# Optimization experiments

Hardware: AMD Instinct MI355X
Metric: run time of the kernel (lower is better)

## Reference

```python
import jax, jax.numpy as jnp
import numpy as np

B, S, H = 4096, 15, 1024
PQ, CFG = 1003, 128
IN = PQ + 5 + 10 + 3 + 3  # 1024, matches input_size in torch module
EPS = 1e-5


def lstm_cell(x, h, c, Wih, Whh, bih, bhh):
    # PyTorch LSTMCell gate order: i, f, g, o
    gates = x @ Wih.T + bih + h @ Whh.T + bhh
    i, f, g, o = jnp.split(gates, 4, axis=-1)
    c2 = jax.nn.sigmoid(f) * c + jax.nn.sigmoid(i) * jnp.tanh(g)
    h2 = jax.nn.sigmoid(o) * jnp.tanh(c2)
    return h2, c2


def setup_inputs() -> dict:
    key = jax.random.key(0)
    ks = jax.random.split(key, 16)
    g = lambda i, shape, s=0.02: jax.random.normal(ks[i], shape, jnp.float32) * s
    u = lambda i, shape: jax.random.uniform(ks[i], shape, jnp.float32, -1.0, 1.0)
    return {
        "input_p_q": jax.random.normal(ks[0], (B, S, PQ), jnp.float32),
        "input_config": jax.random.normal(ks[1], (B, S, CFG), jnp.float32),
        "input_time": jax.random.randint(ks[2], (B, S, 3), 0, 5),
        "W_cfg": g(3, (10, CFG)), "b_cfg": jnp.zeros((10,), jnp.float32),
        "emb_hour": g(4, (24, 5), 1.0),
        "emb_weekday": g(5, (8, 3), 1.0),
        "emb_season": g(6, (5, 3), 1.0),
        # init(): uniform(-1,1) weights, zero bias for the two attention layers
        "W_sa": u(7, (IN, IN + 2 * H)), "b_sa": jnp.zeros((IN,), jnp.float32),
        "Wih_s": g(8, (4 * H, IN)), "Whh_s": g(9, (4 * H, H)),
        "bih_s": jnp.zeros((4 * H,), jnp.float32), "bhh_s": jnp.zeros((4 * H,), jnp.float32),
        "Wih_t": g(10, (4 * H, H)), "Whh_t": g(11, (4 * H, H)),
        "bih_t": jnp.zeros((4 * H,), jnp.float32), "bhh_t": jnp.zeros((4 * H,), jnp.float32),
        "W_ta": u(12, (1, 3 * H)), "b_ta": jnp.zeros((1,), jnp.float32),
        "bn_gamma": jnp.ones((S,), jnp.float32), "bn_beta": jnp.zeros((S,), jnp.float32),
        "Wih_d": g(13, (4, H)), "Whh_d": g(14, (4, 1)),
        "bih_d": jnp.zeros((4,), jnp.float32), "bhh_d": jnp.zeros((4,), jnp.float32),
    }


def reference(input_p_q, input_config, input_time,
              W_cfg, b_cfg, emb_hour, emb_weekday, emb_season,
              W_sa, b_sa, Wih_s, Whh_s, bih_s, bhh_s,
              Wih_t, Whh_t, bih_t, bhh_t, W_ta, b_ta,
              bn_gamma, bn_beta, Wih_d, Whh_d, bih_d, bhh_d):
    cfg = input_config @ W_cfg.T + b_cfg                       # [B,S,10]
    hr = emb_hour[input_time[:, :, 0]]                         # [B,S,5]
    wd = emb_weekday[input_time[:, :, 1]]                      # [B,S,3]
    sn = emb_season[input_time[:, :, 2]]                       # [B,S,3]
    inputs = jnp.concatenate([input_p_q, cfg, hr, wd, sn], axis=2)  # [B,S,IN]

    Bsz, Ssz = inputs.shape[0], inputs.shape[1]
    Hd = Whh_s.shape[1]
    h0 = jnp.zeros((Bsz, Hd), inputs.dtype)

    # ---- spatial encoder with per-step attention gating ----
    def step1(carry, x):
        h, c = carry
        score = jnp.tanh(jnp.concatenate([h, c, x], axis=1) @ W_sa.T + b_sa)
        h2, c2 = lstm_cell(x * score, h, c, Wih_s, Whh_s, bih_s, bhh_s)
        return (h2, c2), h2

    _, mid = jax.lax.scan(step1, (h0, h0), jnp.swapaxes(inputs, 0, 1))  # [S,B,H]
    mid = jnp.swapaxes(mid, 0, 1)                                      # [B,S,H]

    # ---- BatchNorm1d(15) in training mode: channels = sequence dim ----
    mu = mid.mean(axis=(0, 2), keepdims=True)
    var = mid.var(axis=(0, 2), keepdims=True)  # biased variance, as torch uses for normalization
    mid = (mid - mu) * jax.lax.rsqrt(var + EPS) * bn_gamma[None, :, None] + bn_beta[None, :, None]

    # ---- temporal encoder with post-step attention score ----
    def step2(carry, x):
        h, c = carry
        h2, c2 = lstm_cell(x, h, c, Wih_t, Whh_t, bih_t, bhh_t)
        att = jnp.tanh(jnp.concatenate([h2, c2, x], axis=1) @ W_ta.T + b_ta)  # [B,1]
        return (h2, c2), (h2, att)

    _, (outs, att2) = jax.lax.scan(step2, (h0, h0), jnp.swapaxes(mid, 0, 1))
    outs = jnp.swapaxes(outs, 0, 1)   # [B,S,H]
    att2 = jnp.swapaxes(att2, 0, 1)   # [B,S,1]

    # ---- decoder nn.LSTM (batch_first=False!) scans over the BATCH axis ----
    hd0 = jnp.zeros((Ssz, 1), outs.dtype)

    def step3(carry, x):
        h, c = carry
        h2, c2 = lstm_cell(x, h, c, Wih_d, Whh_d, bih_d, bhh_d)
        return (h2, c2), h2

    _, out1d = jax.lax.scan(step3, (hd0, hd0), outs)  # [B,S,1]

    sm = jax.nn.softmax(att2, axis=1)  # [B,S,1]
    # bmm(out1d^T [B,1,S], sm [B,S,1]) -> [B,1,1]
    out = jnp.einsum('bs,bs->b', out1d[:, :, 0], sm[:, :, 0])[:, None, None]
    return out
```

## Files before the change

kernel.cpp:

```cpp
#include <hip/hip_runtime.h>

#define AS1 __attribute__((address_space(1)))
#define AS3 __attribute__((address_space(3)))

typedef __attribute__((ext_vector_type(8))) _Float16 f16x8;
typedef __attribute__((ext_vector_type(4))) float f32x4;

static constexpr int BATCH = 4096;
static constexpr int SEQ   = 15;

__device__ __forceinline__ float h2f(unsigned short u) {
  return (float)__builtin_bit_cast(_Float16, u);
}
__device__ __forceinline__ unsigned short f2h(float f) {
  return __builtin_bit_cast(unsigned short, (_Float16)f);
}
__device__ __forceinline__ float frcp(float x) { return __builtin_amdgcn_rcpf(x); }
__device__ __forceinline__ float sigm(float x)  { return frcp(1.0f + __expf(-x)); }
__device__ __forceinline__ float tanhx(float x) { return 1.0f - 2.0f * frcp(1.0f + __expf(2.0f * x)); }

template<int STAGE>
__global__ __launch_bounds__(512, 2)
void gemm_lstm256(const unsigned short* A0, int lda0, int K0,
                  const unsigned short* A1, int lda1,
                  const unsigned short* Bw, int K,
                  const float* ib, float* Cst,
                  unsigned short* P0, unsigned short* P1, unsigned short* P2,
                  float* F0)
{
  __shared__ unsigned short lds[2][2][16384];
  const int tid  = threadIdx.x;
  const int wid  = tid >> 6;
  const int lane = tid & 63;
  const int wr = wid >> 2;
  const int wc = wid & 3;
  const int NT = K >> 6;

  const int bid = blockIdx.y * gridDim.x + blockIdx.x;
  const int cpx = (gridDim.x * gridDim.y) >> 3;
  const int swz = (bid & 7) * cpx + (bid >> 3);
  const int row0 = (swz / gridDim.x) * 256;
  const int col0 = (swz % gridDim.x) * 256;

  auto stage_half = [&](int bb, int mat, int hh, int kt) {
    const int k0 = kt * 64;
    const unsigned short* Ap; int lda, kc, rb;
    if (mat == 0) {
      if (k0 < K0) { Ap = A0; lda = lda0; kc = k0; }
      else         { Ap = A1; lda = lda1; kc = k0 - K0; }
      rb = row0;
    } else { Ap = Bw; lda = K; kc = k0; rb = col0; }
#pragma unroll
    for (int i = 0; i < 2; ++i) {
      const int x  = (tid + i * 512) * 16;
      const int xs = x ^ (((x >> 9) & 1) << 5);
      const int r  = hh * 128 + (xs >> 7);
      const int cb = xs & 127;
      const unsigned short* src = Ap + (size_t)(rb + r) * lda + kc + (cb >> 1);
      __builtin_amdgcn_global_load_lds((const AS1 void*)src,
          (AS3 void*)((char*)&lds[bb][mat][0] + hh * 16384 + wid * 1024 + i * 8192),
          16, 0, 0);
    }
  };

  const int frow = lane & 15;
  const int axor = ((lane >> 2) & 1) << 5;
  const int abase = ((((wr * 128 + frow) << 7) + (((lane >> 4) & 3) << 4))) ^ axor;
  const int bbase = ((((wc * 64  + frow) << 7) + (((lane >> 4) & 3) << 4))) ^ axor;

  const f32x4 zero = {0.f, 0.f, 0.f, 0.f};
  f32x4 acc[8][4];
#pragma unroll
  for (int i = 0; i < 8; ++i)
#pragma unroll
    for (int j = 0; j < 4; ++j) acc[i][j] = zero;

  stage_half(0, 0, 0, 0);
  stage_half(0, 0, 1, 0);
  stage_half(0, 1, 0, 0);
  stage_half(0, 1, 1, 0);
  if (NT > 1) { stage_half(1, 1, 0, 1); stage_half(1, 1, 1, 1); }
  asm volatile("s_waitcnt vmcnt(4)" ::: "memory");
  __builtin_amdgcn_s_barrier();

#define DO_PHASE(MB, STG, VMW)                                                        \
  {                                                                                   \
    const f16x8 a0 = *(const f16x8*)(ldsA + abase + (MB)     * 2048);                 \
    const f16x8 a1 = *(const f16x8*)(ldsA + abase + (MB)     * 2048 + 64);            \
    const f16x8 a2 = *(const f16x8*)(ldsA + abase + (MB + 1) * 2048);                 \
    const f16x8 a3 = *(const f16x8*)(ldsA + abase + (MB + 1) * 2048 + 64);            \
    STG;                                                                              \
    __builtin_amdgcn_s_barrier();                                                     \
    asm volatile("s_waitcnt lgkmcnt(0)" ::: "memory");                                \
    __builtin_amdgcn_sched_barrier(0);                                                \
    __builtin_amdgcn_s_setprio(1);                                                    \
    _Pragma("unroll")                                                                 \
    for (int n = 0; n < 4; ++n) {                                                     \
      acc[MB][n]     = __builtin_amdgcn_mfma_f32_16x16x32_f16(a0, bv[n][0], acc[MB][n],     0, 0, 0); \
      acc[MB][n]     = __builtin_amdgcn_mfma_f32_16x16x32_f16(a1, bv[n][1], acc[MB][n],     0, 0, 0); \
      acc[MB + 1][n] = __builtin_amdgcn_mfma_f32_16x16x32_f16(a2, bv[n][0], acc[MB + 1][n], 0, 0, 0); \
      acc[MB + 1][n] = __builtin_amdgcn_mfma_f32_16x16x32_f16(a3, bv[n][1], acc[MB + 1][n], 0, 0, 0); \
    }                                                                                 \
    __builtin_amdgcn_s_setprio(0);                                                    \
    VMW;                                                                              \
    __builtin_amdgcn_s_barrier();                                                     \
  }

  for (int kt = 0; kt < NT; ++kt) {
    const int cur = kt & 1;
    const char* ldsA = (const char*)&lds[cur][0][0];
    const char* ldsB = (const char*)&lds[cur][1][0];
    f16x8 bv[4][2];
#pragma unroll
    for (int n = 0; n < 4; ++n) {
      bv[n][0] = *(const f16x8*)(ldsB + bbase + n * 2048);
      bv[n][1] = *(const f16x8*)(ldsB + bbase + n * 2048 + 64);
    }
    DO_PHASE(0, { if (kt + 1 < NT) stage_half(cur ^ 1, 0, 0, kt + 1); }, { (void)0; });
    DO_PHASE(2, { if (kt + 1 < NT) stage_half(cur ^ 1, 0, 1, kt + 1); }, { (void)0; });
    DO_PHASE(4, { if (kt + 2 < NT) stage_half(cur,     1, 0, kt + 2); }, { (void)0; });
    DO_PHASE(6, { if (kt + 2 < NT) stage_half(cur,     1, 1, kt + 2); },
             { if (kt >= NT - 2) { asm volatile("s_waitcnt vmcnt(0)" ::: "memory"); }
               else              { asm volatile("s_waitcnt vmcnt(4)" ::: "memory"); } });
  }
#undef DO_PHASE

  float* xw = ((float*)&lds[0][0][0]) + wid * 256;
  const int cs = lane & 3;
  const int er = (lane >> 4) << 2;
  const int uq = (lane >> 2) & 3;

  float cold[8][4];
#pragma unroll
  for (int mi = 0; mi < 8; ++mi)
#pragma unroll
    for (int ni = 0; ni < 4; ++ni) {
      const int R = row0 + wr * 128 + mi * 16 + er + cs;
      const int U = ((col0 + wc * 64 + ni * 16) >> 2) + uq;
      cold[mi][ni] = Cst[(size_t)R * 1024 + U];
    }

#pragma unroll
  for (int mi = 0; mi < 8; ++mi)
#pragma unroll
    for (int ni = 0; ni < 4; ++ni) {
      __builtin_amdgcn_wave_barrier();
      *(f32x4*)(xw + lane * 4) = acc[mi][ni];
      __builtin_amdgcn_wave_barrier();
      __builtin_amdgcn_sched_barrier(0);
      const int qb = (lane & 60) * 4;
      const float g0 = xw[qb + 0  + cs];
      const float g1 = xw[qb + 4  + cs];
      const float g2 = xw[qb + 8  + cs];
      const float g3 = xw[qb + 12 + cs];
      __builtin_amdgcn_wave_barrier();
      const int R = row0 + wr * 128 + mi * 16 + er + cs;
      const int U = ((col0 + wc * 64 + ni * 16) >> 2) + uq;
      const f32x4 b4 = *(const f32x4*)(ib + 4 * U);
      const float gi = g0 + b4[0];
      const float gf = g1 + b4[1];
      const float gg = g2 + b4[2];
      const float go = g3 + b4[3];
      const size_t off = (size_t)R * 1024 + U;
      const float cn = sigm(gf) * cold[mi][ni] + sigm(gi) * tanhx(gg);
      const float hn = sigm(go) * tanhx(cn);
      Cst[off] = cn;
      const unsigned short hb = f2h(hn);
      if (STAGE == 1) {
        P0[(size_t)R * 2048 + U]        = hb;
        P0[(size_t)R * 2048 + 1024 + U] = f2h(cn);
        P1[(size_t)R * 2048 + 1024 + U] = hb;
        P2[off] = hb;
      } else {
        F0[off] = hn;
        P0[off] = hb;
      }
    }
}

__global__ __launch_bounds__(512, 2)
void gemm_score256(const unsigned short* A0, int lda0, int K0,
                   const unsigned short* A1, int lda1,
                   const unsigned short* Bw, int K,
                   const float* bias, const unsigned short* X,
                   unsigned short* OutG)
{
  __shared__ unsigned short lds[2][24576];
  const int tid  = threadIdx.x;
  const int wid  = tid >> 6;
  const int lane = tid & 63;
  const int wr = wid >> 2;
  const int wc = wid & 3;
  const int NT = K >> 6;

  const int bid = blockIdx.y * gridDim.x + blockIdx.x;
  const int cpx = (gridDim.x * gridDim.y) >> 3;
  const int swz = (bid & 7) * cpx + (bid >> 3);
  const int row0 = (swz / gridDim.x) * 256;
  const int col0 = (swz % gridDim.x) * 128;

  auto stage_half = [&](int bb, int mat, int hh, int kt) {
    const int k0 = kt * 64;
    if (mat == 0) {
      const unsigned short* Ap; int lda, kc;
      if (k0 < K0) { Ap = A0; lda = lda0; kc = k0; }
      else         { Ap = A1; lda = lda1; kc = k0 - K0; }
#pragma unroll
      for (int i = 0; i < 2; ++i) {
        const int x  = (tid + i * 512) * 16;
        const int xs = x ^ (((x >> 9) & 1) << 5);
        const int r  = hh * 128 + (xs >> 7);
        const int cb = xs & 127;
        const unsigned short* src = Ap + (size_t)(row0 + r) * lda + kc + (cb >> 1);
        __builtin_amdgcn_global_load_lds((const AS1 void*)src,
            (AS3 void*)((char*)&lds[bb][0] + hh * 16384 + wid * 1024 + i * 8192),
            16, 0, 0);
      }
    } else {
      const int x  = tid * 16;
      const int xs = x ^ (((x >> 9) & 1) << 5);
      const int r  = hh * 64 + (xs >> 7);
      const int cb = xs & 127;
      const unsigned short* src = Bw + (size_t)(col0 + r) * K + k0 + (cb >> 1);
      __builtin_amdgcn_global_load_lds((const AS1 void*)src,
          (AS3 void*)((char*)&lds[bb][0] + 32768 + hh * 8192 + wid * 1024),
          16, 0, 0);
    }
  };

  const int frow = lane & 15;
  const int axor = ((lane >> 2) & 1) << 5;
  const int abase = ((((wr * 128 + frow) << 7) + (((lane >> 4) & 3) << 4))) ^ axor;
  const int bbase = ((((wc * 32  + frow) << 7) + (((lane >> 4) & 3) << 4))) ^ axor;

  const f32x4 zero = {0.f, 0.f, 0.f, 0.f};
  f32x4 acc[8][2];
#pragma unroll
  for (int i = 0; i < 8; ++i)
#pragma unroll
    for (int j = 0; j < 2; ++j) acc[i][j] = zero;

  stage_half(0, 0, 0, 0);
  stage_half(0, 0, 1, 0);
  stage_half(0, 1, 0, 0);
  stage_half(0, 1, 1, 0);
  if (NT > 1) { stage_half(1, 1, 0, 1); stage_half(1, 1, 1, 1); }
  asm volatile("s_waitcnt vmcnt(2)" ::: "memory");
  __builtin_amdgcn_s_barrier();

#define DO_PHASE_S(MB, STG, VMW)                                                      \
  {                                                                                   \
    const f16x8 a0 = *(const f16x8*)(ldsA + abase + (MB)     * 2048);                 \
    const f16x8 a1 = *(const f16x8*)(ldsA + abase + (MB)     * 2048 + 64);            \
    const f16x8 a2 = *(const f16x8*)(ldsA + abase + (MB + 1) * 2048);                 \
    const f16x8 a3 = *(const f16x8*)(ldsA + abase + (MB + 1) * 2048 + 64);            \
    STG;                                                                              \
    __builtin_amdgcn_s_barrier();                                                     \
    asm volatile("s_waitcnt lgkmcnt(0)" ::: "memory");                                \
    __builtin_amdgcn_sched_barrier(0);                                                \
    __builtin_amdgcn_s_setprio(1);                                                    \
    _Pragma("unroll")                                                                 \
    for (int n = 0; n < 2; ++n) {                                                     \
      acc[MB][n]     = __builtin_amdgcn_mfma_f32_16x16x32_f16(a0, bv[n][0], acc[MB][n],     0, 0, 0); \
      acc[MB][n]     = __builtin_amdgcn_mfma_f32_16x16x32_f16(a1, bv[n][1], acc[MB][n],     0, 0, 0); \
      acc[MB + 1][n] = __builtin_amdgcn_mfma_f32_16x16x32_f16(a2, bv[n][0], acc[MB + 1][n], 0, 0, 0); \
      acc[MB + 1][n] = __builtin_amdgcn_mfma_f32_16x16x32_f16(a3, bv[n][1], acc[MB + 1][n], 0, 0, 0); \
    }                                                                                 \
    __builtin_amdgcn_s_setprio(0);                                                    \
    VMW;                                                                              \
    __builtin_amdgcn_s_barrier();                                                     \
  }

  for (int kt = 0; kt < NT; ++kt) {
    const int cur = kt & 1;
    const char* ldsA = (const char*)&lds[cur][0];
    const char* ldsB = ldsA + 32768;
    f16x8 bv[2][2];
#pragma unroll
    for (int n = 0; n < 2; ++n) {
      bv[n][0] = *(const f16x8*)(ldsB + bbase + n * 2048);
      bv[n][1] = *(const f16x8*)(ldsB + bbase + n * 2048 + 64);
    }
    DO_PHASE_S(0, { if (kt + 1 < NT) stage_half(cur ^ 1, 0, 0, kt + 1); }, { (void)0; });
    DO_PHASE_S(2, { if (kt + 1 < NT) stage_half(cur ^ 1, 0, 1, kt + 1); }, { (void)0; });
    DO_PHASE_S(4, { if (kt + 2 < NT) stage_half(cur,     1, 0, kt + 2); }, { (void)0; });
    DO_PHASE_S(6, { if (kt + 2 < NT) stage_half(cur,     1, 1, kt + 2); },
             { if (kt >= NT - 2) { asm volatile("s_waitcnt vmcnt(0)" ::: "memory"); }
               else              { asm volatile("s_waitcnt vmcnt(2)" ::: "memory"); } });
  }
#undef DO_PHASE_S

  const int er = (lane >> 4) << 2;
#pragma unroll
  for (int mi = 0; mi < 8; ++mi)
#pragma unroll
    for (int ni = 0; ni < 2; ++ni) {
      const int row = row0 + wr * 128 + mi * 16 + er;
      const int col = col0 + wc * 32 + ni * 16 + frow;
      const float bs = bias[col];
#pragma unroll
      for (int r = 0; r < 4; ++r) {
        const float v = tanhx(acc[mi][ni][r] + bs);
        const float xv = h2f(X[(size_t)(row + r) * 1024 + col]);
        OutG[(size_t)(row + r) * 2048 + col] = f2h(xv * v);
      }
    }
}

__global__ void f2h_copy(const float* src, unsigned short* dst, int n) {
  const int i = blockIdx.x * 256 + threadIdx.x;
  if (i < n) dst[i] = f2h(src[i]);
}

__global__ void cat_w_int(const float* wih, const float* whh, unsigned short* dst) {
  const int i = blockIdx.x * 256 + threadIdx.x;
  const int n = i >> 11, k = i & 2047;
  const int u = n >> 2, g = n & 3;
  const int src = g * 1024 + u;
  dst[i] = f2h(k < 1024 ? wih[src * 1024 + k] : whh[src * 1024 + (k - 1024)]);
}

__global__ void prep_bias(const float* bih, const float* bhh, float* ib) {
  const int i = blockIdx.x * 256 + threadIdx.x;
  const int u = i >> 2, g = i & 3;
  ib[i] = bih[g * 1024 + u] + bhh[g * 1024 + u];
}

__global__ void copy_pq(const float* pq, unsigned short* inb) {
  const int i4 = blockIdx.x * 256 + threadIdx.x;
  const float4 v = ((const float4*)pq)[i4];
  const int base = i4 * 4;
  const float vv[4] = {v.x, v.y, v.z, v.w};
#pragma unroll
  for (int e = 0; e < 4; ++e) {
    const int idx = base + e;
    const int bt = idx / 1003;
    const int j = idx - bt * 1003;
    const int b = bt / 15;
    const int t = bt - b * 15;
    inb[((size_t)t * BATCH + b) * 1024 + j] = f2h(vv[e]);
  }
}

__global__ void cfg_emb(const float* cfg, const int* tim,
                        const float* Wc, const float* bc,
                        const float* eh, const float* ew, const float* es,
                        unsigned short* inb)
{
  const int wv = (blockIdx.x * 256 + threadIdx.x) >> 6;
  const int lane = threadIdx.x & 63;
  const int b = wv / 15, t = wv - b * 15;
  const float* cp = cfg + (size_t)wv * 128;
  const float c0 = cp[lane], c1v = cp[lane + 64];
  unsigned short* dst = inb + ((size_t)t * BATCH + b) * 1024;
#pragma unroll
  for (int g = 0; g < 10; ++g) {
    float v = fmaf(c0, Wc[g * 128 + lane], c1v * Wc[g * 128 + 64 + lane]);
    v += __shfl_xor(v, 32); v += __shfl_xor(v, 16); v += __shfl_xor(v, 8);
    v += __shfl_xor(v, 4);  v += __shfl_xor(v, 2);  v += __shfl_xor(v, 1);
    if (lane == 0) dst[1003 + g] = f2h(v + bc[g]);
  }
  if (lane < 5)       dst[1013 + lane] = f2h(eh[tim[wv * 3 + 0] * 5 + lane]);
  else if (lane < 8)  dst[1018 + (lane - 5)] = f2h(ew[tim[wv * 3 + 1] * 3 + (lane - 5)]);
  else if (lane < 11) dst[1021 + (lane - 8)] = f2h(es[tim[wv * 3 + 2] * 3 + (lane - 8)]);
}

__global__ void bn_partial(const unsigned short* mid, float* part) {
  const int t = blockIdx.y, blk = blockIdx.x, tid = threadIdx.x;
  const unsigned short* p = mid + (size_t)t * BATCH * 1024;
  float s = 0.f, ss = 0.f;
  for (int i = blk * 256 + tid; i < BATCH * 1024; i += 128 * 256) {
    const float v = h2f(p[i]);
    s += v; ss += v * v;
  }
  for (int o = 32; o > 0; o >>= 1) { s += __shfl_down(s, o); ss += __shfl_down(ss, o); }
  __shared__ float sm[8];
  if ((tid & 63) == 0) { sm[(tid >> 6) * 2] = s; sm[(tid >> 6) * 2 + 1] = ss; }
  __syncthreads();
  if (tid == 0) {
    part[(t * 128 + blk) * 2]     = sm[0] + sm[2] + sm[4] + sm[6];
    part[(t * 128 + blk) * 2 + 1] = sm[1] + sm[3] + sm[5] + sm[7];
  }
}

__global__ void bn_final(const float* part, const float* gamma, const float* beta, float* scsh) {
  const int t = blockIdx.x, tid = threadIdx.x;
  float s = part[(t * 128 + tid) * 2], ss = part[(t * 128 + tid) * 2 + 1];
  for (int o = 32; o > 0; o >>= 1) { s += __shfl_down(s, o); ss += __shfl_down(ss, o); }
  __shared__ float sm[4];
  if ((tid & 63) == 0) { sm[(tid >> 6) * 2] = s; sm[(tid >> 6) * 2 + 1] = ss; }
  __syncthreads();
  if (tid == 0) {
    const float S = sm[0] + sm[2], SS = sm[1] + sm[3];
    const float inv = 1.f / (float)(BATCH * 1024);
    const float mu = S * inv;
    const float var = SS * inv - mu * mu;
    const float rstd = rsqrtf(var + 1e-5f);
    const float sc = rstd * gamma[t];
    scsh[t * 2] = sc;
    scsh[t * 2 + 1] = beta[t] - mu * sc;
  }
}

__global__ void bn_apply(unsigned short* mid, const float* scsh) {
  const int t = blockIdx.y;
  const int i = blockIdx.x * 256 + threadIdx.x;
  unsigned short* p = mid + (size_t)t * BATCH * 1024;
  p[i] = f2h(h2f(p[i]) * scsh[t * 2] + scsh[t * 2 + 1]);
}

__global__ void att_proj(const float* h2, const float* c2, const unsigned short* xn,
                         const float* Wta, const float* bta, const float* Wihd,
                         float* att2, float* proj, int t)
{
  const int b = blockIdx.x, tid = threadIdx.x;
  const float* h = h2 + (size_t)b * 1024;
  const float* c = c2 + (size_t)b * 1024;
  const unsigned short* x = xn + (size_t)b * 1024;
  float a = 0.f, p0 = 0.f, p1 = 0.f, p2 = 0.f, p3 = 0.f;
  for (int j = tid; j < 1024; j += 256) {
    const float hv = h[j], cv = c[j], xv = h2f(x[j]);
    a  += hv * Wta[j] + cv * Wta[1024 + j] + xv * Wta[2048 + j];
    p0 += hv * Wihd[j];
    p1 += hv * Wihd[1024 + j];
    p2 += hv * Wihd[2048 + j];
    p3 += hv * Wihd[3072 + j];
  }
  for (int o = 32; o > 0; o >>= 1) {
    a  += __shfl_down(a, o);  p0 += __shfl_down(p0, o); p1 += __shfl_down(p1, o);
    p2 += __shfl_down(p2, o); p3 += __shfl_down(p3, o);
  }
  __shared__ float sm[4][5];
  if ((tid & 63) == 0) {
    const int w = tid >> 6;
    sm[w][0] = a; sm[w][1] = p0; sm[w][2] = p1; sm[w][3] = p2; sm[w][4] = p3;
  }
  __syncthreads();
  if (tid == 0) {
    att2[b * SEQ + t] = tanhx(sm[0][0] + sm[1][0] + sm[2][0] + sm[3][0] + bta[0]);
    float* pp = proj + ((size_t)b * SEQ + t) * 4;
    pp[0] = sm[0][1] + sm[1][1] + sm[2][1] + sm[3][1];
    pp[1] = sm[0][2] + sm[1][2] + sm[2][2] + sm[3][2];
    pp[2] = sm[0][3] + sm[1][3] + sm[2][3] + sm[3][3];
    pp[3] = sm[0][4] + sm[1][4] + sm[2][4] + sm[3][4];
  }
}

__global__ __launch_bounds__(256) void lstm3_par(
    const float* proj, const float* Whhd,
    const float* bihd, const float* bhhd, float* out1d)
{
  const int s = blockIdx.x;
  const int tid = threadIdx.x;
  constexpr int CH = BATCH / 256;
  const float wi = Whhd[0], wf = Whhd[1], wg = Whhd[2], wo = Whhd[3];
  const float bi = bihd[0] + bhhd[0], bf_ = bihd[1] + bhhd[1];
  const float bg = bihd[2] + bhhd[2], bo = bihd[3] + bhhd[3];
  const float4* p4 = (const float4*)proj;
  float4 p[CH];
#pragma unroll
  for (int u = 0; u < CH; ++u) p[u] = p4[(tid * CH + u) * SEQ + s];
  __shared__ float Hb[257], Cb[257];
  Hb[tid] = 0.f; Cb[tid] = 0.f;
  if (tid == 255) { Hb[256] = 0.f; Cb[256] = 0.f; }
  __syncthreads();
  float h, c;
  for (int it = 0; it < 8; ++it) {
    h = Hb[tid]; c = Cb[tid];
#pragma unroll
    for (int u = 0; u < CH; ++u) {
      const float gi = fmaf(h, wi, p[u].x + bi);
      const float gf = fmaf(h, wf, p[u].y + bf_);
      const float gg = fmaf(h, wg, p[u].z + bg);
      const float go = fmaf(h, wo, p[u].w + bo);
      c = sigm(gf) * c + sigm(gi) * tanhx(gg);
      h = sigm(go) * tanhx(c);
    }
    __syncthreads();
    Hb[tid + 1] = h; Cb[tid + 1] = c;
    __syncthreads();
  }
  h = Hb[tid]; c = Cb[tid];
#pragma unroll
  for (int u = 0; u < CH; ++u) {
    const float gi = fmaf(h, wi, p[u].x + bi);
    const float gf = fmaf(h, wf, p[u].y + bf_);
    const float gg = fmaf(h, wg, p[u].z + bg);
    const float go = fmaf(h, wo, p[u].w + bo);
    c = sigm(gf) * c + sigm(gi) * tanhx(gg);
    h = sigm(go) * tanhx(c);
    out1d[(tid * CH + u) * SEQ + s] = h;
  }
}

__global__ void finalize_k(const float* att2, const float* out1d, float* out) {
  const int b = blockIdx.x * 64 + threadIdx.x;
  const float* a = att2 + b * SEQ;
  const float* o = out1d + b * SEQ;
  float m = -1e30f;
  for (int s = 0; s < SEQ; ++s) m = fmaxf(m, a[s]);
  float den = 0.f, num = 0.f;
  for (int s = 0; s < SEQ; ++s) {
    const float e = __expf(a[s] - m);
    den += e; num += e * o[s];
  }
  out[b] = num / den;
}

extern "C" void kernel_launch(void* const* d_in, const int* in_sizes, int n_in,
                              void* d_out, int out_size, void* d_ws, size_t ws_size,
                              hipStream_t stream)
{
  (void)in_sizes; (void)n_in; (void)out_size; (void)ws_size;
  const float* in_pq   = (const float*)d_in[0];
  const float* in_cfg  = (const float*)d_in[1];
  const int*   in_time = (const int*)d_in[2];
  const float* W_cfg   = (const float*)d_in[3];
  const float* b_cfg   = (const float*)d_in[4];
  const float* emb_h   = (const float*)d_in[5];
  const float* emb_w   = (const float*)d_in[6];
  const float* emb_s   = (const float*)d_in[7];
  const float* W_sa    = (const float*)d_in[8];
  const float* b_sa    = (const float*)d_in[9];
  const float* Wih_s   = (const float*)d_in[10];
  const float* Whh_s   = (const float*)d_in[11];
  const float* bih_s   = (const float*)d_in[12];
  const float* bhh_s   = (const float*)d_in[13];
  const float* Wih_t   = (const float*)d_in[14];
  const float* Whh_t   = (const float*)d_in[15];
  const float* bih_t   = (const float*)d_in[16];
  const float* bhh_t   = (const float*)d_in[17];
  const float* W_ta    = (const float*)d_in[18];
  const float* b_ta    = (const float*)d_in[19];
  const float* gamma   = (const float*)d_in[20];
  const float* beta    = (const float*)d_in[21];
  const float* Wih_d   = (const float*)d_in[22];
  const float* Whh_d   = (const float*)d_in[23];
  const float* bih_d   = (const float*)d_in[24];
  const float* bhh_d   = (const float*)d_in[25];
  float* out = (float*)d_out;

  char* w = (char*)d_ws;
  size_t off = 0;
  auto alloc = [&](size_t bytes) -> char* {
    char* p = w + off;
    off = (off + bytes + 255) & ~(size_t)255;
    return p;
  };
  unsigned short* inb  = (unsigned short*)alloc((size_t)SEQ * BATCH * 1024 * 2);
  unsigned short* hc   = (unsigned short*)alloc((size_t)BATCH * 2048 * 2);
  unsigned short* gA0  = (unsigned short*)alloc((size_t)BATCH * 2048 * 2);
  unsigned short* gA1  = (unsigned short*)alloc((size_t)BATCH * 2048 * 2);
  float*          c1   = (float*)alloc((size_t)BATCH * 1024 * 4);
  unsigned short* h2b0 = (unsigned short*)alloc((size_t)BATCH * 1024 * 2);
  unsigned short* h2b1 = (unsigned short*)alloc((size_t)BATCH * 1024 * 2);
  float*          h2f_ = (float*)alloc((size_t)BATCH * 1024 * 4);
  float*          c2f  = (float*)alloc((size_t)BATCH * 1024 * 4);
  unsigned short* wsab = (unsigned short*)alloc((size_t)1024 * 3072 * 2);
  unsigned short* w1   = (unsigned short*)alloc((size_t)4096 * 2048 * 2);
  unsigned short* w2   = (unsigned short*)alloc((size_t)4096 * 2048 * 2);
  float*          ib1  = (float*)alloc(4096 * 4);
  float*          ib2  = (float*)alloc(4096 * 4);
  float*          part = (float*)alloc(15 * 128 * 2 * 4);
  float*          scsh = (float*)alloc(15 * 2 * 4);
  float*          att2 = (float*)alloc((size_t)BATCH * SEQ * 4);
  float*          proj = (float*)alloc((size_t)BATCH * SEQ * 4 * 4);
  float*          o1d  = (float*)alloc((size_t)BATCH * SEQ * 4);

  unsigned short* gAbuf[2]  = {gA0, gA1};
  unsigned short* h2bbuf[2] = {h2b0, h2b1};

  hipMemsetAsync(hc,   0, (size_t)BATCH * 2048 * 2, stream);
  hipMemsetAsync(gA0,  0, (size_t)BATCH * 2048 * 2, stream);
  hipMemsetAsync(c1,   0, (size_t)BATCH * 1024 * 4, stream);
  hipMemsetAsync(h2b0, 0, (size_t)BATCH * 1024 * 2, stream);
  hipMemsetAsync(c2f,  0, (size_t)BATCH * 1024 * 4, stream);

  f2h_copy<<<(1024 * 3072) / 256, 256, 0, stream>>>(W_sa, wsab, 1024 * 3072);
  cat_w_int<<<(4096 * 2048) / 256, 256, 0, stream>>>(Wih_s, Whh_s, w1);
  cat_w_int<<<(4096 * 2048) / 256, 256, 0, stream>>>(Wih_t, Whh_t, w2);
  prep_bias<<<16, 256, 0, stream>>>(bih_s, bhh_s, ib1);
  prep_bias<<<16, 256, 0, stream>>>(bih_t, bhh_t, ib2);
  copy_pq<<<(BATCH * SEQ * 1003 / 4) / 256, 256, 0, stream>>>(in_pq, inb);
  cfg_emb<<<(BATCH * SEQ) / 4, 256, 0, stream>>>(in_cfg, in_time, W_cfg, b_cfg,
                                                 emb_h, emb_w, emb_s, inb);

  for (int t = 0; t < SEQ; ++t) {
    unsigned short* xt = inb + (size_t)t * BATCH * 1024;
    gemm_score256<<<dim3(1024 / 128, BATCH / 256), 512, 0, stream>>>(
        hc, 2048, 2048, xt, 1024, wsab, 3072, b_sa, xt, gAbuf[t & 1]);
    gemm_lstm256<1><<<dim3(4096 / 256, BATCH / 256), 512, 0, stream>>>(
        gAbuf[t & 1], 2048, 2048, gAbuf[t & 1], 2048, w1, 2048,
        ib1, c1, hc, gAbuf[(t + 1) & 1], xt, nullptr);
  }

  bn_partial<<<dim3(128, SEQ), 256, 0, stream>>>(inb, part);
  bn_final<<<SEQ, 128, 0, stream>>>(part, gamma, beta, scsh);
  bn_apply<<<dim3((BATCH * 1024) / 256, SEQ), 256, 0, stream>>>(inb, scsh);

  for (int t = 0; t < SEQ; ++t) {
    const unsigned short* xt = inb + (size_t)t * BATCH * 1024;
    gemm_lstm256<2><<<dim3(4096 / 256, BATCH / 256), 512, 0, stream>>>(
        xt, 1024, 1024, h2bbuf[t & 1], 1024, w2, 2048,
        ib2, c2f, h2bbuf[(t + 1) & 1], nullptr, nullptr, h2f_);
    att_proj<<<BATCH, 256, 0, stream>>>(h2f_, c2f, xt, W_ta, b_ta, Wih_d, att2, proj, t);
  }

  lstm3_par<<<SEQ, 256, 0, stream>>>(proj, Whh_d, bih_d, bhh_d, o1d);
  finalize_k<<<BATCH / 64, 64, 0, stream>>>(att2, o1d, out);
}
```

Before: 4.206 ms.

## Stage LSTM epilogue through LDS for coalesced stores; shrink score GEMM tiles

The LSTM GEMM epilogue now writes h and c into shared memory, then copies them out with 16-byte coalesced row stores instead of scattered 2-byte stores to several output buffers. The score GEMM moves from 256x128 tiles with 512 threads to 128x64 tiles with 256 threads, in a simpler two-phase pipeline. That gives four times as many blocks, which should fill the GPU better. The cost is an extra block barrier and LDS round trip in the epilogue, and less operand reuse per score tile.

```diff
diff --git a/kernel.cpp b/kernel.cpp
--- a/kernel.cpp
+++ b/kernel.cpp
@@ -125,7 +125,13 @@
   }
 #undef DO_PHASE
 
-  float* xw = ((float*)&lds[0][0][0]) + wid * 256;
+  __syncthreads();
+  char* base = (char*)&lds[0][0][0];
+  unsigned short* hS = (unsigned short*)base;
+  unsigned short* cS = (unsigned short*)(base + 32768);
+  float*          hF = (float*)base;
+  float* xw = (float*)(base + 65536) + wid * 256;
+
   const int cs = lane & 3;
   const int er = (lane >> 4) << 2;
   const int uq = (lane >> 2) & 3;
@@ -161,141 +167,173 @@
       const float gf = g1 + b4[1];
       const float gg = g2 + b4[2];
       const float go = g3 + b4[3];
-      const size_t off = (size_t)R * 1024 + U;
       const float cn = sigm(gf) * cold[mi][ni] + sigm(gi) * tanhx(gg);
       const float hn = sigm(go) * tanhx(cn);
-      Cst[off] = cn;
-      const unsigned short hb = f2h(hn);
+      Cst[(size_t)R * 1024 + U] = cn;
+      const int Rl = wr * 128 + mi * 16 + er + cs;
+      const int Ul = wc * 16 + ni * 4 + uq;
       if (STAGE == 1) {
-        P0[(size_t)R * 2048 + U]        = hb;
-        P0[(size_t)R * 2048 + 1024 + U] = f2h(cn);
-        P1[(size_t)R * 2048 + 1024 + U] = hb;
-        P2[off] = hb;
+        hS[Rl * 64 + Ul] = f2h(hn);
+        cS[Rl * 64 + Ul] = f2h(cn);
       } else {
-        F0[off] = hn;
-        P0[off] = hb;
+        hF[Rl * 64 + Ul] = hn;
       }
     }
-}
-
-__global__ __launch_bounds__(512, 2)
-void gemm_score256(const unsigned short* A0, int lda0, int K0,
+  __syncthreads();
+
+  const int U0 = col0 >> 2;
+  if (STAGE == 1) {
+#pragma unroll
+    for (int it = 0; it < 4; ++it) {
+      const int idx = it * 512 + tid;
+      const int r = idx >> 3, o = idx & 7;
+      const int4 hv = *(const int4*)((char*)hS + idx * 16);
+      const int4 cv = *(const int4*)((char*)cS + idx * 16);
+      *(int4*)(P0 + (size_t)(row0 + r) * 2048 + U0 + o * 8)        = hv;
+      *(int4*)(P0 + (size_t)(row0 + r) * 2048 + 1024 + U0 + o * 8) = cv;
+      *(int4*)(P1 + (size_t)(row0 + r) * 2048 + 1024 + U0 + o * 8) = hv;
+      *(int4*)(P2 + (size_t)(row0 + r) * 1024 + U0 + o * 8)        = hv;
+    }
+  } else {
+#pragma unroll
+    for (int it = 0; it < 8; ++it) {
+      const int idx = it * 512 + tid;
+      const int r = idx >> 4, o = idx & 15;
+      const f32x4 hv = *(const f32x4*)((char*)hF + idx * 16);
+      *(f32x4*)(F0 + (size_t)(row0 + r) * 1024 + U0 + o * 4) = hv;
+      uint2 pk;
+      pk.x = (unsigned)f2h(hv[0]) | ((unsigned)f2h(hv[1]) << 16);
+      pk.y = (unsigned)f2h(hv[2]) | ((unsigned)f2h(hv[3]) << 16);
+      *(uint2*)(P0 + (size_t)(row0 + r) * 1024 + U0 + o * 4) = pk;
+    }
+  }
+}
+
+__global__ __launch_bounds__(256, 2)
+void gemm_score2ph(const unsigned short* A0, int lda0, int K0,
                    const unsigned short* A1, int lda1,
                    const unsigned short* Bw, int K,
                    const float* bias, const unsigned short* X,
                    unsigned short* OutG)
 {
-  __shared__ unsigned short lds[2][24576];
+  __shared__ unsigned short lds[2][12288];
   const int tid  = threadIdx.x;
   const int wid  = tid >> 6;
   const int lane = tid & 63;
-  const int wr = wid >> 2;
-  const int wc = wid & 3;
+  const int wr = wid >> 1;
+  const int wc = wid & 1;
   const int NT = K >> 6;
 
   const int bid = blockIdx.y * gridDim.x + blockIdx.x;
   const int cpx = (gridDim.x * gridDim.y) >> 3;
   const int swz = (bid & 7) * cpx + (bid >> 3);
-  const int row0 = (swz / gridDim.x) * 256;
-  const int col0 = (swz % gridDim.x) * 128;
-
-  auto stage_half = [&](int bb, int mat, int hh, int kt) {
+  const int row0 = (swz / gridDim.x) * 128;
+  const int col0 = (swz % gridDim.x) * 64;
+
+  auto stage_A = [&](int bb, int kt) {
     const int k0 = kt * 64;
-    if (mat == 0) {
-      const unsigned short* Ap; int lda, kc;
-      if (k0 < K0) { Ap = A0; lda = lda0; kc = k0; }
-      else         { Ap = A1; lda = lda1; kc = k0 - K0; }
-#pragma unroll
-      for (int i = 0; i < 2; ++i) {
-        const int x  = (tid + i * 512) * 16;
-        const int xs = x ^ (((x >> 9) & 1) << 5);
-        const int r  = hh * 128 + (xs >> 7);
-        const int cb = xs & 127;
-        const unsigned short* src = Ap + (size_t)(row0 + r) * lda + kc + (cb >> 1);
-        __builtin_amdgcn_global_load_lds((const AS1 void*)src,
-            (AS3 void*)((char*)&lds[bb][0] + hh * 16384 + wid * 1024 + i * 8192),
-            16, 0, 0);
-      }
-    } else {
-      const int x  = tid * 16;
+    const unsigned short* Ap; int lda, kc;
+    if (k0 < K0) { Ap = A0; lda = lda0; kc = k0; }
+    else         { Ap = A1; lda = lda1; kc = k0 - K0; }
+#pragma unroll
+    for (int i = 0; i < 4; ++i) {
+      const int x  = (i * 256 + tid) * 16;
       const int xs = x ^ (((x >> 9) & 1) << 5);
-      const int r  = hh * 64 + (xs >> 7);
+      const int r  = xs >> 7;
+      const int cb = xs & 127;
+      const unsigned short* src = Ap + (size_t)(row0 + r) * lda + kc + (cb >> 1);
+      __builtin_amdgcn_global_load_lds((const AS1 void*)src,
+          (AS3 void*)((char*)&lds[bb][0] + i * 4096 + wid * 1024), 16, 0, 0);
+    }
+  };
+  auto stage_B = [&](int bb, int kt) {
+    const int k0 = kt * 64;
+#pragma unroll
+    for (int i = 0; i < 2; ++i) {
+      const int x  = (i * 256 + tid) * 16;
+      const int xs = x ^ (((x >> 9) & 1) << 5);
+      const int r  = xs >> 7;
       const int cb = xs & 127;
       const unsigned short* src = Bw + (size_t)(col0 + r) * K + k0 + (cb >> 1);
       __builtin_amdgcn_global_load_lds((const AS1 void*)src,
-          (AS3 void*)((char*)&lds[bb][0] + 32768 + hh * 8192 + wid * 1024),
-          16, 0, 0);
+          (AS3 void*)((char*)&lds[bb][0] + 16384 + i * 4096 + wid * 1024), 16, 0, 0);
     }
   };
 
   const int frow = lane & 15;
   const int axor = ((lane >> 2) & 1) << 5;
-  const int abase = ((((wr * 128 + frow) << 7) + (((lane >> 4) & 3) << 4))) ^ axor;
-  const int bbase = ((((wc * 32  + frow) << 7) + (((lane >> 4) & 3) << 4))) ^ axor;
+  const int abase = ((((wr * 64 + frow) << 7) + ((lane >> 4) << 4))) ^ axor;
+  const int bbase = ((((wc * 32 + frow) << 7) + ((lane >> 4) << 4))) ^ axor;
 
   const f32x4 zero = {0.f, 0.f, 0.f, 0.f};
-  f32x4 acc[8][2];
-#pragma unroll
-  for (int i = 0; i < 8; ++i)
+  f32x4 acc[4][2];
+#pragma unroll
+  for (int i = 0; i < 4; ++i)
 #pragma unroll
     for (int j = 0; j < 2; ++j) acc[i][j] = zero;
 
-  stage_half(0, 0, 0, 0);
-  stage_half(0, 0, 1, 0);
-  stage_half(0, 1, 0, 0);
-  stage_half(0, 1, 1, 0);
-  if (NT > 1) { stage_half(1, 1, 0, 1); stage_half(1, 1, 1, 1); }
+  stage_A(0, 0);
+  stage_B(0, 0);
+  if (NT > 1) stage_B(1, 1);
   asm volatile("s_waitcnt vmcnt(2)" ::: "memory");
   __builtin_amdgcn_s_barrier();
-
-#define DO_PHASE_S(MB, STG, VMW)                                                      \
-  {                                                                                   \
-    const f16x8 a0 = *(const f16x8*)(ldsA + abase + (MB)     * 2048);                 \
-    const f16x8 a1 = *(const f16x8*)(ldsA + abase + (MB)     * 2048 + 64);            \
-    const f16x8 a2 = *(const f16x8*)(ldsA + abase + (MB + 1) * 2048);                 \
-    const f16x8 a3 = *(const f16x8*)(ldsA + abase + (MB + 1) * 2048 + 64);            \
-    STG;                                                                              \
-    __builtin_amdgcn_s_barrier();                                                     \
-    asm volatile("s_waitcnt lgkmcnt(0)" ::: "memory");                                \
-    __builtin_amdgcn_sched_barrier(0);                                                \
-    __builtin_amdgcn_s_setprio(1);                                                    \
-    _Pragma("unroll")                                                                 \
-    for (int n = 0; n < 2; ++n) {                                                     \
-      acc[MB][n]     = __builtin_amdgcn_mfma_f32_16x16x32_f16(a0, bv[n][0], acc[MB][n],     0, 0, 0); \
-      acc[MB][n]     = __builtin_amdgcn_mfma_f32_16x16x32_f16(a1, bv[n][1], acc[MB][n],     0, 0, 0); \
-      acc[MB + 1][n] = __builtin_amdgcn_mfma_f32_16x16x32_f16(a2, bv[n][0], acc[MB + 1][n], 0, 0, 0); \
-      acc[MB + 1][n] = __builtin_amdgcn_mfma_f32_16x16x32_f16(a3, bv[n][1], acc[MB + 1][n], 0, 0, 0); \
-    }                                                                                 \
-    __builtin_amdgcn_s_setprio(0);                                                    \
-    VMW;                                                                              \
-    __builtin_amdgcn_s_barrier();                                                     \
-  }
 
   for (int kt = 0; kt < NT; ++kt) {
     const int cur = kt & 1;
     const char* ldsA = (const char*)&lds[cur][0];
-    const char* ldsB = ldsA + 32768;
+    const char* ldsB = ldsA + 16384;
     f16x8 bv[2][2];
 #pragma unroll
     for (int n = 0; n < 2; ++n) {
       bv[n][0] = *(const f16x8*)(ldsB + bbase + n * 2048);
       bv[n][1] = *(const f16x8*)(ldsB + bbase + n * 2048 + 64);
     }
-    DO_PHASE_S(0, { if (kt + 1 < NT) stage_half(cur ^ 1, 0, 0, kt + 1); }, { (void)0; });
-    DO_PHASE_S(2, { if (kt + 1 < NT) stage_half(cur ^ 1, 0, 1, kt + 1); }, { (void)0; });
-    DO_PHASE_S(4, { if (kt + 2 < NT) stage_half(cur,     1, 0, kt + 2); }, { (void)0; });
-    DO_PHASE_S(6, { if (kt + 2 < NT) stage_half(cur,     1, 1, kt + 2); },
-             { if (kt >= NT - 2) { asm volatile("s_waitcnt vmcnt(0)" ::: "memory"); }
-               else              { asm volatile("s_waitcnt vmcnt(2)" ::: "memory"); } });
-  }
-#undef DO_PHASE_S
+    f16x8 a00 = *(const f16x8*)(ldsA + abase);
+    f16x8 a01 = *(const f16x8*)(ldsA + abase + 64);
+    f16x8 a10 = *(const f16x8*)(ldsA + abase + 2048);
+    f16x8 a11 = *(const f16x8*)(ldsA + abase + 2048 + 64);
+    if (kt + 1 < NT) stage_A(cur ^ 1, kt + 1);
+    __builtin_amdgcn_s_barrier();
+    asm volatile("s_waitcnt lgkmcnt(0)" ::: "memory");
+    __builtin_amdgcn_sched_barrier(0);
+    __builtin_amdgcn_s_setprio(1);
+#pragma unroll
+    for (int n = 0; n < 2; ++n) {
+      acc[0][n] = __builtin_amdgcn_mfma_f32_16x16x32_f16(a00, bv[n][0], acc[0][n], 0, 0, 0);
+      acc[0][n] = __builtin_amdgcn_mfma_f32_16x16x32_f16(a01, bv[n][1], acc[0][n], 0, 0, 0);
+      acc[1][n] = __builtin_amdgcn_mfma_f32_16x16x32_f16(a10, bv[n][0], acc[1][n], 0, 0, 0);
+      acc[1][n] = __builtin_amdgcn_mfma_f32_16x16x32_f16(a11, bv[n][1], acc[1][n], 0, 0, 0);
+    }
+    __builtin_amdgcn_s_setprio(0);
+    __builtin_amdgcn_s_barrier();
+    f16x8 a20 = *(const f16x8*)(ldsA + abase + 2 * 2048);
+    f16x8 a21 = *(const f16x8*)(ldsA + abase + 2 * 2048 + 64);
+    f16x8 a30 = *(const f16x8*)(ldsA + abase + 3 * 2048);
+    f16x8 a31 = *(const f16x8*)(ldsA + abase + 3 * 2048 + 64);
+    if (kt + 2 < NT) stage_B(cur, kt + 2);
+    __builtin_amdgcn_s_barrier();
+    asm volatile("s_waitcnt lgkmcnt(0)" ::: "memory");
+    __builtin_amdgcn_sched_barrier(0);
+    __builtin_amdgcn_s_setprio(1);
+#pragma unroll
+    for (int n = 0; n < 2; ++n) {
+      acc[2][n] = __builtin_amdgcn_mfma_f32_16x16x32_f16(a20, bv[n][0], acc[2][n], 0, 0, 0);
+      acc[2][n] = __builtin_amdgcn_mfma_f32_16x16x32_f16(a21, bv[n][1], acc[2][n], 0, 0, 0);
+      acc[3][n] = __builtin_amdgcn_mfma_f32_16x16x32_f16(a30, bv[n][0], acc[3][n], 0, 0, 0);
+      acc[3][n] = __builtin_amdgcn_mfma_f32_16x16x32_f16(a31, bv[n][1], acc[3][n], 0, 0, 0);
+    }
+    __builtin_amdgcn_s_setprio(0);
+    if (kt >= NT - 2) { asm volatile("s_waitcnt vmcnt(0)" ::: "memory"); }
+    else              { asm volatile("s_waitcnt vmcnt(2)" ::: "memory"); }
+    __builtin_amdgcn_s_barrier();
+  }
 
   const int er = (lane >> 4) << 2;
 #pragma unroll
-  for (int mi = 0; mi < 8; ++mi)
+  for (int mi = 0; mi < 4; ++mi)
 #pragma unroll
     for (int ni = 0; ni < 2; ++ni) {
-      const int row = row0 + wr * 128 + mi * 16 + er;
+      const int row = row0 + wr * 64 + mi * 16 + er;
       const int col = col0 + wc * 32 + ni * 16 + frow;
       const float bs = bias[col];
 #pragma unroll
@@ -587,7 +625,7 @@
 
   for (int t = 0; t < SEQ; ++t) {
     unsigned short* xt = inb + (size_t)t * BATCH * 1024;
-    gemm_score256<<<dim3(1024 / 128, BATCH / 256), 512, 0, stream>>>(
+    gemm_score2ph<<<dim3(1024 / 64, BATCH / 128), 256, 0, stream>>>(
         hc, 2048, 2048, xt, 1024, wsab, 3072, b_sa, xt, gAbuf[t & 1]);
     gemm_lstm256<1><<<dim3(4096 / 256, BATCH / 256), 512, 0, stream>>>(
         gAbuf[t & 1], 2048, 2048, gAbuf[t & 1], 2048, w1, 2048,
```

After: 3.544 ms. -15.7%, faster.
